# Performance work log

Measured on AMD Instinct MI355X. Metric: run time of the kernel, lower is better.

The kernel has to match this reference:

```python
import jax, jax.numpy as jnp
import numpy as np

MUL = 32          # multiplicity per irrep
NB = 10           # number_of_basis
MAX_R = 4.0
NUM_NEIGH = 16.0
NUM_NODES = 512.0
N_GRAPHS = 16
N = 8192
E = 131072
L = 3             # gated layers
C_S = float(np.sin(np.pi / 8))
C_X = float(np.cos(np.pi / 8))
SQ3 = float(np.sqrt(3.0))
SQ2 = float(np.sqrt(2.0))


def smooth_cutoff(x):
    u = 2.0 * (x - 1.0)
    y = 0.5 * (1.0 - jnp.cos(np.pi * u))
    return jnp.where(u > 0.0, 0.0, jnp.where(u < -1.0, 1.0, y))


def radial_embed(r):
    # soft_one_hot_linspace, basis='gaussian', cutoff=False, scaled by sqrt(NB)
    values = jnp.linspace(0.0, MAX_R, NB)
    step = values[1] - values[0]
    diff = (r[:, None] - values[None, :]) / step
    return jnp.exp(-diff * diff) / 1.12 * np.sqrt(NB)


def _lin_s(a, w):  # scalar-channel linear with e3nn fan-in norm
    return (a @ w) / np.sqrt(w.shape[0])


def _lin_v(a, w):  # vector-channel (l=1) linear, acts on multiplicity only
    return jnp.einsum('nui,uv->nvi', a, w) / np.sqrt(w.shape[0])


def forward(x, edge_vec, lin1_so, lin1_se, lin1_vo, lin1_ve,
            sc_so, sc_se, sc_vo, sc_ve, rad_w1, rad_w2,
            lin2_so, lin2_se, lin2_vo, lin2_ve,
            flin1_se, flin1_vo, fsc_se, frad_w1, frad_w2, flin2,
            edge_src, edge_dst, batch):
    n = x.shape[0]
    M = MUL
    # split node features into irrep blocks: 32x0o + 32x0e + 32x1o + 32x1e
    s_o = x[:, :M]
    s_e = x[:, M:2 * M]
    v_o = x[:, 2 * M:5 * M].reshape(n, M, 3)
    v_e = x[:, 5 * M:8 * M].reshape(n, M, 3)

    r = jnp.linalg.norm(edge_vec, axis=1)
    unit = edge_vec / (r[:, None] + 1e-12)
    cut = smooth_cutoff(r / MAX_R)          # [E]
    y0 = cut                                # l=0 edge attr (Y0 = 1, component norm)
    y1 = SQ3 * unit * cut[:, None]          # l=1 edge attr, [E,3]
    emb = radial_embed(r)                   # [E,NB]

    def seg(v):
        return jax.ops.segment_sum(v, edge_dst, num_segments=n) / np.sqrt(NUM_NEIGH)

    inv2 = 1.0 / np.sqrt(2.0)  # path normalization: 2 tp paths into output irrep
    inv3 = 1.0 / np.sqrt(3.0)  # 3 tp paths into output irrep

    def layer(carry, p):
        s_o, s_e, v_o, v_e = carry
        (w1so, w1se, w1vo, w1ve, wsso, wsse, wsvo, wsve,
         rw1, rw2, w2so, w2se, w2vo, w2ve) = p
        # lin1 (FullyConnectedTensorProduct with trivial node attr == per-irrep linear)
        a_so, a_se = _lin_s(s_o, w1so), _lin_s(s_e, w1se)
        a_vo, a_ve = _lin_v(v_o, w1vo), _lin_v(v_e, w1ve)
        e_so, e_se = a_so[edge_src], a_se[edge_src]
        e_vo, e_ve = a_vo[edge_src], a_ve[edge_src]
        # radial MLP -> per-edge tensor-product weights (10 uvu paths x MUL)
        h = jax.nn.silu(emb @ rw1 / np.sqrt(NB))
        w = (h @ rw2 / np.sqrt(rw1.shape[1])).reshape(-1, 10, M)
        # explicit lmax=1 Clebsch-Gordan contractions
        dot_ve = jnp.einsum('eui,ei->eu', e_ve, y1) / SQ3   # 1e x 1o -> 0o
        dot_vo = jnp.einsum('eui,ei->eu', e_vo, y1) / SQ3   # 1o x 1o -> 0e
        cr_ve = jnp.cross(e_ve, y1[:, None, :]) / SQ2       # 1e x 1o -> 1o
        cr_vo = jnp.cross(e_vo, y1[:, None, :]) / SQ2       # 1o x 1o -> 1e
        m0o = jnp.concatenate([w[:, 0] * e_so * y0[:, None],
                               w[:, 1] * dot_ve], axis=1) * inv2          # [E,2M]
        m0e = jnp.concatenate([w[:, 2] * e_se * y0[:, None],
                               w[:, 3] * dot_vo], axis=1) * inv2          # [E,2M]
        m1o = jnp.concatenate([w[:, 4][:, :, None] * e_se[:, :, None] * y1[:, None, :],
                               w[:, 5][:, :, None] * e_vo * y0[:, None, None],
                               w[:, 6][:, :, None] * cr_ve], axis=1) * inv3  # [E,3M,3]
        m1e = jnp.concatenate([w[:, 7][:, :, None] * e_so[:, :, None] * y1[:, None, :],
                               w[:, 8][:, :, None] * cr_vo,
                               w[:, 9][:, :, None] * e_ve * y0[:, None, None]], axis=1) * inv3
        n0o, n0e, n1o, n1e = seg(m0o), seg(m0e), seg(m1o), seg(m1e)
        # lin2 plus self-connection skip: sin(pi/8)*sc + cos(pi/8)*conv
        o0o = C_S * _lin_s(s_o, wsso) + C_X * _lin_s(n0o, w2so)   # [N,M]
        o0e = C_S * _lin_s(s_e, wsse) + C_X * _lin_s(n0e, w2se)   # [N,3M] (M scalars + 2M gates)
        o1o = C_S * _lin_v(v_o, wsvo) + C_X * _lin_v(n1o, w2vo)   # [N,M,3]
        o1e = C_S * _lin_v(v_e, wsve) + C_X * _lin_v(n1e, w2ve)   # [N,M,3]
        # Gate: tanh on 0o scalars, silu on 0e scalars, sigmoid gates on vectors
        ns_o = jnp.tanh(o0o)
        ns_e = jax.nn.silu(o0e[:, :M])
        g = jax.nn.sigmoid(o0e[:, M:])
        nv_o = o1o * g[:, :M, None]
        nv_e = o1e * g[:, M:, None]
        return (ns_o, ns_e, nv_o, nv_e), None

    (s_o, s_e, v_o, v_e), _ = jax.lax.scan(
        layer, (s_o, s_e, v_o, v_e),
        (lin1_so, lin1_se, lin1_vo, lin1_ve, sc_so, sc_se, sc_vo, sc_ve,
         rad_w1, rad_w2, lin2_so, lin2_se, lin2_vo, lin2_ve))

    # final convolution -> 1x0e (paths: 0e x 0e -> 0e, 1o x 1o -> 0e)
    a_se = _lin_s(s_e, flin1_se)
    a_vo = _lin_v(v_o, flin1_vo)
    h = jax.nn.silu(emb @ frad_w1 / np.sqrt(NB))
    w = (h @ frad_w2 / np.sqrt(frad_w1.shape[1])).reshape(-1, 2, MUL)
    dot_vo = jnp.einsum('eui,ei->eu', a_vo[edge_src], y1) / SQ3
    m0e = jnp.concatenate([w[:, 0] * a_se[edge_src] * y0[:, None],
                           w[:, 1] * dot_vo], axis=1) * inv2
    n0e = seg(m0e)
    out = C_S * _lin_s(s_e, fsc_se) + C_X * _lin_s(n0e, flin2)   # [N,1]
    # reduce_output: per-graph sum / sqrt(num_nodes)
    return jax.ops.segment_sum(out, batch, num_segments=N_GRAPHS) / np.sqrt(NUM_NODES)


def setup_inputs():
    key = jax.random.key(0)
    ks = jax.random.split(key, 26)
    rn = lambda k, s: jax.random.normal(k, s, dtype=jnp.float32)
    M = MUL
    return {
        "x": rn(ks[0], (N, 8 * M)),
        "edge_vec": rn(ks[1], (E, 3)),
        "lin1_so": rn(ks[2], (L, M, M)),
        "lin1_se": rn(ks[3], (L, M, M)),
        "lin1_vo": rn(ks[4], (L, M, M)),
        "lin1_ve": rn(ks[5], (L, M, M)),
        "sc_so": rn(ks[6], (L, M, M)),
        "sc_se": rn(ks[7], (L, M, 3 * M)),
        "sc_vo": rn(ks[8], (L, M, M)),
        "sc_ve": rn(ks[9], (L, M, M)),
        "rad_w1": rn(ks[10], (L, NB, 100)),
        "rad_w2": rn(ks[11], (L, 100, 10 * M)),
        "lin2_so": rn(ks[12], (L, 2 * M, M)),
        "lin2_se": rn(ks[13], (L, 2 * M, 3 * M)),
        "lin2_vo": rn(ks[14], (L, 3 * M, M)),
        "lin2_ve": rn(ks[15], (L, 3 * M, M)),
        "flin1_se": rn(ks[16], (M, M)),
        "flin1_vo": rn(ks[17], (M, M)),
        "fsc_se": rn(ks[18], (M, 1)),
        "frad_w1": rn(ks[19], (NB, 100)),
        "frad_w2": rn(ks[20], (100, 2 * M)),
        "flin2": rn(ks[21], (2 * M, 1)),
        "edge_src": jax.random.randint(ks[22], (E,), 0, N),
        "edge_dst": jax.random.randint(ks[23], (E,), 0, N),
        "batch": jnp.sort(jax.random.randint(ks[24], (N,), 0, N_GRAPHS)),
    }


def reference(x, edge_vec, lin1_so, lin1_se, lin1_vo, lin1_ve,
              sc_so, sc_se, sc_vo, sc_ve, rad_w1, rad_w2,
              lin2_so, lin2_se, lin2_vo, lin2_ve,
              flin1_se, flin1_vo, fsc_se, frad_w1, frad_w2, flin2,
              edge_src, edge_dst, batch):
    return forward(x, edge_vec, lin1_so, lin1_se, lin1_vo, lin1_ve,
                   sc_so, sc_se, sc_vo, sc_ve, rad_w1, rad_w2,
                   lin2_so, lin2_se, lin2_vo, lin2_ve,
                   flin1_se, flin1_vo, fsc_se, frad_w1, frad_w2, flin2,
                   edge_src, edge_dst, batch)
```

## Files before the change

kernel.cpp:

```cpp
#include <hip/hip_runtime.h>
#include <hip/hip_bf16.h>
#include <math.h>
#include <string.h>
#include <stdint.h>

#define NN 8192
#define EE 131072

#define PI_F     3.14159265358979323846f
#define SQRT3_F  1.7320508075688772f
#define INV_SQ2  0.7071067811865476f
#define INV_SQ3  0.5773502691896258f
#define INV_S32  0.17677669529663687f
#define INV_S96  0.10206207261596575f
#define INV_S10  0.31622776601683794f
#define C_S_F    0.3826834323650898f
#define C_X_F    0.9238795325112867f
#define EMB_S    2.8234621965789795f
#define OUT_S    0.044194173824159216f

typedef unsigned int uint;
typedef unsigned short ushort;
typedef unsigned long long u64;
typedef __attribute__((ext_vector_type(8))) short short8;
typedef __attribute__((ext_vector_type(4))) float float4v;

__device__ __forceinline__ float sigmoid_f(float x){ return 1.0f/(1.0f+__expf(-x)); }
__device__ __forceinline__ ushort f2bf(float f){
    uint u = __float_as_uint(f);
    u = (u + 0x7fffu + ((u>>16)&1u)) >> 16;
    return (ushort)u;
}
__device__ __forceinline__ float bf2f(ushort w){ return __uint_as_float(((uint)w)<<16); }
__device__ __forceinline__ uint pk2bf(float a, float b){
    __hip_bfloat162 h = __float22bfloat162_rn(make_float2(a,b));
    uint u; memcpy(&u,&h,4); return u;
}

__global__ __launch_bounds__(256) void k_count(const int* __restrict__ dst, int* __restrict__ cnt)
{
    int e = blockIdx.x*256 + threadIdx.x;
    atomicAdd(&cnt[dst[e]], 1);
}

__global__ __launch_bounds__(1024) void k_scan(const int* __restrict__ cnt,
    int* __restrict__ off, int* __restrict__ cur)
{
    __shared__ int partial[1024];
    int t = threadIdx.x;
    int base = t*8;
    int local[8];
    int s = 0;
    #pragma unroll
    for(int i=0;i<8;i++){ local[i]=s; s += cnt[base+i]; }
    partial[t] = s;
    __syncthreads();
    for(int d=1; d<1024; d<<=1){
        int v = (t>=d) ? partial[t-d] : 0;
        __syncthreads();
        partial[t] += v;
        __syncthreads();
    }
    int pref = (t>0) ? partial[t-1] : 0;
    #pragma unroll
    for(int i=0;i<8;i++){
        int o = pref + local[i];
        off[base+i] = o; cur[base+i] = o;
    }
    if (t==1023) off[NN] = partial[1023];
}

__global__ __launch_bounds__(256) void k_scatter(const int* __restrict__ dst,
    int* __restrict__ cur, int* __restrict__ eids)
{
    int e = blockIdx.x*256 + threadIdx.x;
    int p = atomicAdd(&cur[dst[e]], 1);
    eids[p] = e;
}

__global__ __launch_bounds__(256) void k_geom_sorted(const float* __restrict__ ev,
    const int* __restrict__ eids, const int* __restrict__ esrc,
    const int* __restrict__ edst, const int* __restrict__ batch,
    float* __restrict__ y0s, float* __restrict__ y1s, float* __restrict__ embs,
    int* __restrict__ esrcs, int* __restrict__ gbs)
{
    int p = blockIdx.x*256 + threadIdx.x;
    int e = eids[p];
    float vx=ev[e*3+0], vy=ev[e*3+1], vz=ev[e*3+2];
    float r = sqrtf(vx*vx+vy*vy+vz*vz);
    float uu = 0.5f*r - 2.0f;
    float cut;
    if (uu > 0.0f)       cut = 0.0f;
    else if (uu < -1.0f) cut = 1.0f;
    else                 cut = 0.5f*(1.0f - cosf(PI_F*uu));
    y0s[p] = cut;
    float s = SQRT3_F*cut/(r + 1e-12f);
    y1s[p*3+0]=vx*s; y1s[p*3+1]=vy*s; y1s[p*3+2]=vz*s;
    #pragma unroll
    for(int b=0;b<10;b++){
        float d = r*2.25f - (float)b;
        embs[p*10+b] = __expf(-d*d)*EMB_S;
    }
    esrcs[p] = esrc[e];
    gbs[p]   = batch[edst[e]];
}

__global__ __launch_bounds__(256) void k_lin1(const float* __restrict__ st,
    const float* __restrict__ w_so, const float* __restrict__ w_se,
    const float* __restrict__ w_vo, const float* __restrict__ w_ve,
    float* __restrict__ A)
{
    __shared__ float wl[4][1024];
    __shared__ float sl[8][256];
    int t = threadIdx.x;
    for(int i=t;i<1024;i+=256){ wl[0][i]=w_so[i]; wl[1][i]=w_se[i]; wl[2][i]=w_vo[i]; wl[3][i]=w_ve[i]; }
    int n0 = blockIdx.x*8;
    for(int i=t;i<2048;i+=256){ int k=i>>8, c=i&255; sl[k][c]=st[(n0+k)*256+c]; }
    __syncthreads();
    for(int k=0;k<8;k++){
        float acc = 0.0f;
        if (t < 64){
            int m = t>>5, v = t&31;
            const float* w = wl[m];
            const float* s = &sl[k][m*32];
            #pragma unroll
            for(int u=0;u<32;u++) acc += s[u]*w[u*32+v];
        } else if (t < 160){
            int idx=t-64, i=idx>>5, v=idx&31;
            #pragma unroll
            for(int u=0;u<32;u++) acc += sl[k][64+u*3+i]*wl[2][u*32+v];
        } else {
            int idx=t-160, i=idx>>5, v=idx&31;
            #pragma unroll
            for(int u=0;u<32;u++) acc += sl[k][160+u*3+i]*wl[3][u*32+v];
        }
        A[(n0+k)*256 + t] = acc * INV_S32;
    }
}

__global__ __launch_bounds__(256) void k_prep3(const float* __restrict__ rw2, ushort* __restrict__ Bfrag)
{
    int L = blockIdx.x / 160;
    int idx = (blockIdx.x % 160)*256 + threadIdx.x;
    int j = idx & 7;
    int l = (idx>>3) & 63;
    int rest = idx >> 9;
    int nt = rest % 20;
    int ks = rest / 20;
    int k = ks*32 + ((l>>4)&3)*8 + j;
    int p = nt*16 + (l&15);
    int n = (p % 10)*32 + p/10;
    float v = (k < 100) ? rw2[L*32000 + k*320 + n] : 0.0f;
    Bfrag[L*40960 + idx] = f2bf(v);
}

__global__ __launch_bounds__(256) void k_prep64(const float* __restrict__ rw2, ushort* __restrict__ Bfrag)
{
    int idx = blockIdx.x*256 + threadIdx.x;
    int j = idx & 7;
    int l = (idx>>3) & 63;
    int rest = idx >> 9;
    int nt = rest % 4;
    int ks = rest / 4;
    int k = ks*32 + ((l>>4)&3)*8 + j;
    int p = nt*16 + (l&15);
    int n = (p % 2)*32 + p/2;
    float v = (k < 100) ? rw2[k*64 + n] : 0.0f;
    Bfrag[idx] = f2bf(v);
}

__global__ __launch_bounds__(256) void k_prepu(
    const float* __restrict__ sc_so, const float* __restrict__ sc_se,
    const float* __restrict__ sc_vo, const float* __restrict__ sc_ve,
    const float* __restrict__ lin2_so, const float* __restrict__ lin2_se,
    const float* __restrict__ lin2_vo, const float* __restrict__ lin2_ve,
    float* __restrict__ Wcat0, float* __restrict__ Wcat1)
{
    int idx = blockIdx.x*256 + threadIdx.x;
    int L = idx / 20480;
    int k = idx % 20480;
    const float CS32 = C_S_F*INV_S32, CX8 = C_X_F*0.125f, CX96 = C_X_F*INV_S96;
    if (k < 12288){
        int r = k >> 7, c = k & 127;
        float v;
        if (c < 32) v = (r<32) ? CS32*sc_so[L*1024 + r*32+c]        : CX8*lin2_so[L*2048 + (r-32)*32+c];
        else        v = (r<32) ? CS32*sc_se[L*3072 + r*96+(c-32)]   : CX8*lin2_se[L*6144 + (r-32)*96+(c-32)];
        Wcat0[L*12288 + k] = v;
    } else {
        int k2 = k - 12288;
        int r = k2 >> 6, c = k2 & 63;
        float v;
        if (c < 32) v = (r<32) ? CS32*sc_vo[L*1024 + r*32+c]        : CX96*lin2_vo[L*3072 + (r-32)*32+c];
        else        v = (r<32) ? CS32*sc_ve[L*1024 + r*32+(c-32)]   : CX96*lin2_ve[L*3072 + (r-32)*32+(c-32)];
        Wcat1[L*8192 + k2] = v;
    }
}

template<int NCOL>
__global__ __launch_bounds__(256, 3) void k_radial_mfma(const float* __restrict__ emb,
    const float* __restrict__ rw1, const ushort* __restrict__ Afrag,
    ushort* __restrict__ Wout)
{
    constexpr int MTW = NCOL/64;
    __shared__ __align__(16) ushort s_frag[8192];
    __shared__ float s_emb[640];
    int t = threadIdx.x;
    int ebase = blockIdx.x*64;
    for(int i=t;i<640;i+=256)  s_emb[i] = emb[ebase*10 + i];
    for(int i=t;i<1024;i+=256) ((uint*)s_frag)[3072 + i] = 0u;
    __syncthreads();
    {
        int w4 = __builtin_amdgcn_readfirstlane(t) >> 6;
        int l = t & 63;
        float ev[10];
        #pragma unroll
        for(int r=0;r<10;r++) ev[r] = s_emb[l*10 + r];
        int m  = l & 15, nt = l >> 4;
        int kbeg = w4*25;
        #pragma unroll 5
        for(int k=kbeg; k<kbeg+25; k++){
            float a0 = 0.0f;
            #pragma unroll
            for(int r=0;r<10;r++) a0 += ev[r]*rw1[r*100 + k];
            a0 *= INV_S10;
            float h = a0*sigmoid_f(a0);
            int ks = k >> 5, kk = k & 31;
            int lt = m | ((kk>>3)<<4);
            s_frag[((ks*4 + nt)*64 + lt)*8 + (kk&7)] = f2bf(h);
        }
    }
    __syncthreads();
    int w = t >> 6, l = t & 63;
    float4v acc[MTW][4];
    #pragma unroll
    for(int a=0;a<MTW;a++)
        #pragma unroll
        for(int b=0;b<4;b++)
            acc[a][b] = (float4v){0.f,0.f,0.f,0.f};
    #pragma unroll
    for(int ks=0;ks<4;ks++){
        short8 bfr[4];
        #pragma unroll
        for(int nt=0;nt<4;nt++)
            bfr[nt] = *((const short8*)&s_frag[((ks*4+nt)*64 + l)*8]);
        #pragma unroll
        for(int mtl=0;mtl<MTW;mtl++){
            short8 af = *((const short8*)(Afrag + ((size_t)(ks*(NCOL/16) + w*MTW + mtl)*64 + l)*8));
            #pragma unroll
            for(int nt=0;nt<4;nt++)
                acc[mtl][nt] = __builtin_amdgcn_mfma_f32_16x16x32_bf16(af, bfr[nt], acc[mtl][nt], 0, 0, 0);
        }
    }
    {
        int col16 = l & 15, rquad = l >> 4;
        #pragma unroll
        for(int mtl=0;mtl<MTW;mtl++){
            int pos0 = (w*MTW + mtl)*16 + rquad*4;
            #pragma unroll
            for(int nt=0;nt<4;nt++){
                int edge = ebase + nt*16 + col16;
                uint u01 = pk2bf(acc[mtl][nt][0]*0.1f, acc[mtl][nt][1]*0.1f);
                uint u23 = pk2bf(acc[mtl][nt][2]*0.1f, acc[mtl][nt][3]*0.1f);
                u64 pk = (u64)u01 | ((u64)u23 << 32);
                *((u64*)(Wout + (size_t)edge*NCOL + pos0)) = pk;
            }
        }
    }
}

__global__ __launch_bounds__(256) void k_aggregate(const float* __restrict__ A,
    const ushort* __restrict__ W2, const float* __restrict__ y0s,
    const float* __restrict__ y1s, const int* __restrict__ off,
    const int* __restrict__ esrcs, float* __restrict__ nbuf)
{
    int t = threadIdx.x;
    int n = blockIdx.x*4 + (t >> 6);
    int l = t & 63;
    int u = l & 31, half = l >> 5;
    int e0 = off[n], e1 = off[n+1];
    float a_n0o0=0.f, a_n0o1=0.f, a_n0e0=0.f, a_n0e1=0.f;
    float a1o[3][3] = {{0}}, a1e[3][3] = {{0}};
    #pragma unroll 2
    for(int p=e0;p<e1;p+=2){
        int idx = p + half;
        bool valid = idx < e1;
        int ic = valid ? idx : e0;
        int s = esrcs[ic];
        float cy0 = valid ? y0s[ic] : 0.0f;
        float v1x = y1s[ic*3+0], v1y = y1s[ic*3+1], v1z = y1s[ic*3+2];
        if (!valid){ v1x=0.f; v1y=0.f; v1z=0.f; }
        const float* Ar = A + s*256;
        float aso=Ar[u],      ase=Ar[32+u];
        float vox=Ar[64+u],   voy=Ar[96+u],  voz=Ar[128+u];
        float vex=Ar[160+u],  vey=Ar[192+u], vez=Ar[224+u];
        const uint* Wr = (const uint*)(W2 + (size_t)ic*320 + u*10);
        uint p01=Wr[0], p23=Wr[1], p45=Wr[2], p67=Wr[3], p89=Wr[4];
        float w0=bf2f((ushort)p01), w1=bf2f((ushort)(p01>>16));
        float w2=bf2f((ushort)p23), w3=bf2f((ushort)(p23>>16));
        float w4=bf2f((ushort)p45), w5=bf2f((ushort)(p45>>16));
        float w6=bf2f((ushort)p67), w7=bf2f((ushort)(p67>>16));
        float w8=bf2f((ushort)p89), w9=bf2f((ushort)(p89>>16));
        float dve = (vex*v1x+vey*v1y+vez*v1z)*INV_SQ3;
        float dvo = (vox*v1x+voy*v1y+voz*v1z)*INV_SQ3;
        float cvex=(vey*v1z-vez*v1y)*INV_SQ2, cvey=(vez*v1x-vex*v1z)*INV_SQ2, cvez=(vex*v1y-vey*v1x)*INV_SQ2;
        float cvox=(voy*v1z-voz*v1y)*INV_SQ2, cvoy=(voz*v1x-vox*v1z)*INV_SQ2, cvoz=(vox*v1y-voy*v1x)*INV_SQ2;
        a_n0o0 += w0*aso*cy0;
        a_n0o1 += w1*dve;
        a_n0e0 += w2*ase*cy0;
        a_n0e1 += w3*dvo;
        a1o[0][0]+=w4*ase*v1x; a1o[0][1]+=w4*ase*v1y; a1o[0][2]+=w4*ase*v1z;
        a1o[1][0]+=w5*vox*cy0; a1o[1][1]+=w5*voy*cy0; a1o[1][2]+=w5*voz*cy0;
        a1o[2][0]+=w6*cvex;    a1o[2][1]+=w6*cvey;    a1o[2][2]+=w6*cvez;
        a1e[0][0]+=w7*aso*v1x; a1e[0][1]+=w7*aso*v1y; a1e[0][2]+=w7*aso*v1z;
        a1e[1][0]+=w8*cvox;    a1e[1][1]+=w8*cvoy;    a1e[1][2]+=w8*cvoz;
        a1e[2][0]+=w9*vex*cy0; a1e[2][1]+=w9*vey*cy0; a1e[2][2]+=w9*vez*cy0;
    }
    a_n0o0 += __shfl_xor(a_n0o0, 32);
    a_n0o1 += __shfl_xor(a_n0o1, 32);
    a_n0e0 += __shfl_xor(a_n0e0, 32);
    a_n0e1 += __shfl_xor(a_n0e1, 32);
    #pragma unroll
    for(int sp=0;sp<3;sp++)
        #pragma unroll
        for(int i=0;i<3;i++){
            a1o[sp][i] += __shfl_xor(a1o[sp][i], 32);
            a1e[sp][i] += __shfl_xor(a1e[sp][i], 32);
        }
    float s0 = INV_SQ2*0.25f;
    float s1 = INV_SQ3*0.25f;
    float* nb = nbuf + n*704;
    if (half==0){
        nb[u]      = a_n0o0*s0;
        nb[32+u]   = a_n0o1*s0;
        nb[64+u]   = a_n0e0*s0;
        nb[96+u]   = a_n0e1*s0;
        #pragma unroll
        for(int sp=0;sp<3;sp++)
            #pragma unroll
            for(int i=0;i<3;i++)
                nb[128 + i*96 + sp*32 + u] = a1o[sp][i]*s1;
    } else {
        #pragma unroll
        for(int sp=0;sp<3;sp++)
            #pragma unroll
            for(int i=0;i<3;i++)
                nb[416 + i*96 + sp*32 + u] = a1e[sp][i]*s1;
    }
}

__global__ __launch_bounds__(256, 4) void k_update(const float* __restrict__ st,
    const float* __restrict__ nbuf, const float* __restrict__ W0,
    const float* __restrict__ W1, float* __restrict__ stnew)
{
    __shared__ float X0T[192][8];
    __shared__ float X1T[3][256][8];
    __shared__ float G[8][64];
    int t = threadIdx.x;
    int n0 = blockIdx.x*8;
    for (int idx=t; idx<2048; idx+=256){
        int nb = idx>>8, c = idx&255;
        float v = st[(n0+nb)*256 + c];
        if (c<32)       X0T[c][nb]=v;
        else if (c<64)  X0T[96+(c-32)][nb]=v;
        else if (c<160){ int cc=c-64;  X1T[cc%3][cc/3][nb]=v; }
        else           { int cc=c-160; X1T[cc%3][128+cc/3][nb]=v; }
    }
    for (int idx=t; idx<5632; idx+=256){
        int nb = idx/704, o = idx%704;
        float v = nbuf[(n0+nb)*704 + o];
        if (o<64)       X0T[32+o][nb]=v;
        else if (o<128) X0T[128+(o-64)][nb]=v;
        else if (o<416){ int oo=o-128; X1T[oo/96][32+(oo%96)][nb]=v; }
        else           { int oo=o-416; X1T[oo/96][160+(oo%96)][nb]=v; }
    }
    __syncthreads();
    {
        int c = t & 127, h = t >> 7;
        float a0=0.f,a1=0.f,a2=0.f,a3=0.f;
        int qb = (c<32) ? 0 : 96;
        #pragma unroll 4
        for (int r=0;r<96;r++){
            float w = W0[r*128+c];
            const float* xp = &X0T[qb+r][h*4];
            a0 += w*xp[0]; a1 += w*xp[1]; a2 += w*xp[2]; a3 += w*xp[3];
        }
        float accs[4]={a0,a1,a2,a3};
        #pragma unroll
        for (int j=0;j<4;j++){
            int nb = h*4+j, n = n0+nb;
            float o = accs[j];
            if (c<32)       stnew[n*256+c] = tanhf(o);
            else if (c<64)  stnew[n*256+c] = o*sigmoid_f(o);
            else            G[nb][c-64] = sigmoid_f(o);
        }
    }
    __syncthreads();
    int c2 = t & 63, w = t >> 6;
    if (w < 3){
        float acc[8];
        #pragma unroll
        for(int j=0;j<8;j++) acc[j]=0.f;
        int qb = (c2<32) ? 0 : 128;
        #pragma unroll 2
        for (int r=0;r<128;r++){
            float wt = W1[r*64+c2];
            const float* xp = &X1T[w][qb+r][0];
            #pragma unroll
            for(int j=0;j<8;j++) acc[j] += wt*xp[j];
        }
        int base = (c2<32) ? 64 + c2*3 + w : 160 + (c2-32)*3 + w;
        #pragma unroll
        for(int j=0;j<8;j++)
            stnew[(n0+j)*256 + base] = acc[j]*G[j][c2];
    }
}

__global__ __launch_bounds__(128) void k_flin(const float* __restrict__ st,
    const float* __restrict__ wse, const float* __restrict__ wvo,
    const float* __restrict__ fsc_se,
    float* __restrict__ afin, float* __restrict__ sk)
{
    int n = blockIdx.x, t = threadIdx.x;
    const float* sr = st + n*256;
    float acc = 0.0f;
    if (t < 32){
        #pragma unroll
        for(int u=0;u<32;u++) acc += sr[32+u]*wse[u*32+t];
    } else {
        int idx=t-32, i=idx>>5, v=idx&31;
        #pragma unroll
        for(int u=0;u<32;u++) acc += sr[64+u*3+i]*wvo[u*32+v];
    }
    afin[n*128 + t] = acc * INV_S32;
    if (t < 32){
        float v = sr[32+t]*fsc_se[t];
        #pragma unroll
        for(int o=16;o>0;o>>=1) v += __shfl_xor(v, o);
        if (t==0) sk[n] = v * (C_S_F*INV_S32*OUT_S);
    }
}

__global__ __launch_bounds__(256) void k_fagg(const float* __restrict__ afin,
    const ushort* __restrict__ Wf2, const int* __restrict__ esrcs,
    const float* __restrict__ y0s, const float* __restrict__ y1s,
    const int* __restrict__ gbs, const float* __restrict__ flin2,
    float* __restrict__ fpart)
{
    __shared__ float s_g[16];
    int t = threadIdx.x;
    if (t < 16) s_g[t] = 0.0f;
    __syncthreads();
    int u = t & 31, half = (t>>5)&1, w = t >> 6;
    const float FACT = C_X_F*0.125f*INV_SQ2*0.25f*OUT_S;
    float fl0 = flin2[u], fl1 = flin2[32+u];
    int base = (blockIdx.x*4 + w)*64;
    #pragma unroll 2
    for(int it=0; it<32; it++){
        int idx = base + it*2 + half;
        int s = esrcs[idx];
        float cy0 = y0s[idx];
        float v1x=y1s[idx*3+0], v1y=y1s[idx*3+1], v1z=y1s[idx*3+2];
        const float* Ar = afin + s*128;
        float ase = Ar[u];
        float vx=Ar[32+u], vy=Ar[64+u], vz=Ar[96+u];
        uint p01 = *((const uint*)(Wf2 + (size_t)idx*64 + u*2));
        float w0 = bf2f((ushort)p01), w1 = bf2f((ushort)(p01>>16));
        float val = fl0*w0*ase*cy0 + fl1*w1*((vx*v1x+vy*v1y+vz*v1z)*INV_SQ3);
        #pragma unroll
        for(int o=16;o>0;o>>=1) val += __shfl_xor(val, o);
        if (u==0) atomicAdd(&s_g[gbs[idx]], val*FACT);
    }
    __syncthreads();
    if (t < 16) fpart[blockIdx.x*16 + t] = s_g[t];
}

__global__ __launch_bounds__(256) void k_final(const float* __restrict__ sk,
    const int* __restrict__ batch, const float* __restrict__ fpart,
    float* __restrict__ out)
{
    __shared__ float bins[16];
    int t = threadIdx.x, b = blockIdx.x;
    if (t < 16) bins[t] = 0.0f;
    __syncthreads();
    if (t < 128){
        int n = b*128 + t;
        atomicAdd(&bins[batch[n]], sk[n]);
    } else {
        int i = b*128 + (t-128);
        atomicAdd(&bins[i & 15], fpart[i]);
    }
    __syncthreads();
    if (t < 16) atomicAdd(&out[t], bins[t]);
}

extern "C" void kernel_launch(void* const* d_in, const int* in_sizes, int n_in,
                              void* d_out, int out_size, void* d_ws, size_t ws_size,
                              hipStream_t stream)
{
    const float* x        = (const float*)d_in[0];
    const float* edge_vec = (const float*)d_in[1];
    const float* lin1_so  = (const float*)d_in[2];
    const float* lin1_se  = (const float*)d_in[3];
    const float* lin1_vo  = (const float*)d_in[4];
    const float* lin1_ve  = (const float*)d_in[5];
    const float* sc_so    = (const float*)d_in[6];
    const float* sc_se    = (const float*)d_in[7];
    const float* sc_vo    = (const float*)d_in[8];
    const float* sc_ve    = (const float*)d_in[9];
    const float* rad_w1   = (const float*)d_in[10];
    const float* rad_w2   = (const float*)d_in[11];
    const float* lin2_so  = (const float*)d_in[12];
    const float* lin2_se  = (const float*)d_in[13];
    const float* lin2_vo  = (const float*)d_in[14];
    const float* lin2_ve  = (const float*)d_in[15];
    const float* flin1_se = (const float*)d_in[16];
    const float* flin1_vo = (const float*)d_in[17];
    const float* fsc_se   = (const float*)d_in[18];
    const float* frad_w1  = (const float*)d_in[19];
    const float* frad_w2  = (const float*)d_in[20];
    const float* flin2    = (const float*)d_in[21];
    const int*   esrc     = (const int*)d_in[22];
    const int*   edst     = (const int*)d_in[23];
    const int*   batch    = (const int*)d_in[24];
    float* out = (float*)d_out;

    uint8_t* ws = (uint8_t*)d_ws;
    size_t off = 0;
    auto alloc = [&](size_t bytes)->void* {
        void* p = ws + off;
        off += (bytes + 255) & ~(size_t)255;
        return p;
    };
    float* y0s   = (float*)alloc((size_t)EE*4);
    float* y1s   = (float*)alloc((size_t)EE*12);
    float* embs  = (float*)alloc((size_t)EE*40);
    int*   esrcs = (int*)  alloc((size_t)EE*4);
    int*   gbs   = (int*)  alloc((size_t)EE*4);
    int*   cnt   = (int*)  alloc((size_t)NN*4);
    int*   csro  = (int*)  alloc((size_t)(NN+1)*4);
    int*   cur   = (int*)  alloc((size_t)NN*4);
    int*   eids  = (int*)  alloc((size_t)EE*4);
    float* A     = (float*)alloc((size_t)NN*256*4);
    ushort* W    = (ushort*)alloc((size_t)EE*320*2);
    ushort* Bfrag3=(ushort*)alloc((size_t)3*40960*2);
    ushort* BfragF=(ushort*)alloc((size_t)8192*2);
    float* Wcat0 = (float*)alloc((size_t)3*12288*4);
    float* Wcat1 = (float*)alloc((size_t)3*8192*4);
    float* nbuf  = (float*)alloc((size_t)NN*704*4);
    float* st0   = (float*)alloc((size_t)NN*256*4);
    float* st1   = (float*)alloc((size_t)NN*256*4);
    float* afin  = (float*)alloc((size_t)NN*128*4);
    float* sk    = (float*)alloc((size_t)NN*4);
    float* fpart = (float*)alloc((size_t)512*16*4);

    hipMemsetAsync(out, 0, (size_t)out_size*sizeof(float), stream);
    hipMemsetAsync(cnt, 0, (size_t)NN*4, stream);

    k_count  <<<EE/256, 256, 0, stream>>>(edst, cnt);
    k_scan   <<<1, 1024, 0, stream>>>(cnt, csro, cur);
    k_scatter<<<EE/256, 256, 0, stream>>>(edst, cur, eids);
    k_geom_sorted<<<EE/256, 256, 0, stream>>>(edge_vec, eids, esrc, edst, batch,
                                              y0s, y1s, embs, esrcs, gbs);
    k_prep3<<<480, 256, 0, stream>>>(rad_w2, Bfrag3);
    k_prep64<<<32, 256, 0, stream>>>(frad_w2, BfragF);
    k_prepu<<<240, 256, 0, stream>>>(sc_so, sc_se, sc_vo, sc_ve,
                                     lin2_so, lin2_se, lin2_vo, lin2_ve, Wcat0, Wcat1);

    const float* st_in = x;
    float* bufs[2] = { st0, st1 };
    for (int l=0; l<3; l++){
        k_lin1<<<NN/8, 256, 0, stream>>>(st_in,
            lin1_so + l*1024, lin1_se + l*1024, lin1_vo + l*1024, lin1_ve + l*1024, A);
        k_radial_mfma<320><<<EE/64, 256, 0, stream>>>(embs, rad_w1 + l*1000, Bfrag3 + l*40960, W);
        k_aggregate<<<NN/4, 256, 0, stream>>>(A, W, y0s, y1s, csro, esrcs, nbuf);
        float* st_out = bufs[l & 1];
        k_update<<<NN/8, 256, 0, stream>>>(st_in, nbuf, Wcat0 + l*12288, Wcat1 + l*8192, st_out);
        st_in = st_out;
    }
    k_flin<<<NN, 128, 0, stream>>>(st_in, flin1_se, flin1_vo, fsc_se, afin, sk);
    k_radial_mfma<64><<<EE/64, 256, 0, stream>>>(embs, frad_w1, BfragF, W);
    k_fagg<<<512, 256, 0, stream>>>(afin, W, esrcs, y0s, y1s, gbs, flin2, fpart);
    k_final<<<64, 256, 0, stream>>>(sk, batch, fpart, out);
}
```

Measured before the change: 578.0 us.

## Pack edge geometry into float4 and permute radial weight layout for coalescing

Edge geometry (cutoff plus the three l=1 components) is merged into one float4 per edge, so the aggregate and final-aggregate kernels issue a single vector load instead of four scalar loads. The column permutation in the radial weight prep is changed so each edge's per-channel bf16 weight pairs are laid out channel-contiguous, and the aggregate kernel's five weight loads become coalesced across lanes instead of strided by 10. The aggregate kernel also moves to one 64-thread block per node instead of four nodes per 256-thread block, which may help balance uneven degrees but adds more, smaller blocks.

Result: no change. 583.8 us (+1.0%).

```diff
diff --git a/kernel.cpp b/kernel.cpp
--- a/kernel.cpp
+++ b/kernel.cpp
@@ -81,7 +81,7 @@
 __global__ __launch_bounds__(256) void k_geom_sorted(const float* __restrict__ ev,
     const int* __restrict__ eids, const int* __restrict__ esrc,
     const int* __restrict__ edst, const int* __restrict__ batch,
-    float* __restrict__ y0s, float* __restrict__ y1s, float* __restrict__ embs,
+    float4* __restrict__ ygeo, float* __restrict__ embs,
     int* __restrict__ esrcs, int* __restrict__ gbs)
 {
     int p = blockIdx.x*256 + threadIdx.x;
@@ -93,9 +93,8 @@
     if (uu > 0.0f)       cut = 0.0f;
     else if (uu < -1.0f) cut = 1.0f;
     else                 cut = 0.5f*(1.0f - cosf(PI_F*uu));
-    y0s[p] = cut;
     float s = SQRT3_F*cut/(r + 1e-12f);
-    y1s[p*3+0]=vx*s; y1s[p*3+1]=vy*s; y1s[p*3+2]=vz*s;
+    ygeo[p] = make_float4(cut, vx*s, vy*s, vz*s);
     #pragma unroll
     for(int b=0;b<10;b++){
         float d = r*2.25f - (float)b;
@@ -149,7 +148,7 @@
     int ks = rest / 20;
     int k = ks*32 + ((l>>4)&3)*8 + j;
     int p = nt*16 + (l&15);
-    int n = (p % 10)*32 + p/10;
+    int n = (2*(p>>6) + (p&1))*32 + ((p&63)>>1);
     float v = (k < 100) ? rw2[L*32000 + k*320 + n] : 0.0f;
     Bfrag[L*40960 + idx] = f2bf(v);
 }
@@ -268,14 +267,13 @@
     }
 }
 
-__global__ __launch_bounds__(256) void k_aggregate(const float* __restrict__ A,
-    const ushort* __restrict__ W2, const float* __restrict__ y0s,
-    const float* __restrict__ y1s, const int* __restrict__ off,
-    const int* __restrict__ esrcs, float* __restrict__ nbuf)
-{
-    int t = threadIdx.x;
-    int n = blockIdx.x*4 + (t >> 6);
-    int l = t & 63;
+__global__ __launch_bounds__(64) void k_aggregate(const float* __restrict__ A,
+    const ushort* __restrict__ W2, const float4* __restrict__ ygeo,
+    const int* __restrict__ off, const int* __restrict__ esrcs,
+    float* __restrict__ nbuf)
+{
+    int n = blockIdx.x;
+    int l = threadIdx.x;
     int u = l & 31, half = l >> 5;
     int e0 = off[n], e1 = off[n+1];
     float a_n0o0=0.f, a_n0o1=0.f, a_n0e0=0.f, a_n0e1=0.f;
@@ -286,15 +284,16 @@
         bool valid = idx < e1;
         int ic = valid ? idx : e0;
         int s = esrcs[ic];
-        float cy0 = valid ? y0s[ic] : 0.0f;
-        float v1x = y1s[ic*3+0], v1y = y1s[ic*3+1], v1z = y1s[ic*3+2];
+        float4 yg = ygeo[ic];
+        float cy0 = valid ? yg.x : 0.0f;
+        float v1x = yg.y, v1y = yg.z, v1z = yg.w;
         if (!valid){ v1x=0.f; v1y=0.f; v1z=0.f; }
         const float* Ar = A + s*256;
         float aso=Ar[u],      ase=Ar[32+u];
         float vox=Ar[64+u],   voy=Ar[96+u],  voz=Ar[128+u];
         float vex=Ar[160+u],  vey=Ar[192+u], vez=Ar[224+u];
-        const uint* Wr = (const uint*)(W2 + (size_t)ic*320 + u*10);
-        uint p01=Wr[0], p23=Wr[1], p45=Wr[2], p67=Wr[3], p89=Wr[4];
+        const uint* Wu = (const uint*)(W2) + (size_t)ic*160;
+        uint p01=Wu[u], p23=Wu[32+u], p45=Wu[64+u], p67=Wu[96+u], p89=Wu[128+u];
         float w0=bf2f((ushort)p01), w1=bf2f((ushort)(p01>>16));
         float w2=bf2f((ushort)p23), w3=bf2f((ushort)(p23>>16));
         float w4=bf2f((ushort)p45), w5=bf2f((ushort)(p45>>16));
@@ -442,9 +441,8 @@
 
 __global__ __launch_bounds__(256) void k_fagg(const float* __restrict__ afin,
     const ushort* __restrict__ Wf2, const int* __restrict__ esrcs,
-    const float* __restrict__ y0s, const float* __restrict__ y1s,
-    const int* __restrict__ gbs, const float* __restrict__ flin2,
-    float* __restrict__ fpart)
+    const float4* __restrict__ ygeo, const int* __restrict__ gbs,
+    const float* __restrict__ flin2, float* __restrict__ fpart)
 {
     __shared__ float s_g[16];
     int t = threadIdx.x;
@@ -458,14 +456,13 @@
     for(int it=0; it<32; it++){
         int idx = base + it*2 + half;
         int s = esrcs[idx];
-        float cy0 = y0s[idx];
-        float v1x=y1s[idx*3+0], v1y=y1s[idx*3+1], v1z=y1s[idx*3+2];
+        float4 yg = ygeo[idx];
         const float* Ar = afin + s*128;
         float ase = Ar[u];
         float vx=Ar[32+u], vy=Ar[64+u], vz=Ar[96+u];
         uint p01 = *((const uint*)(Wf2 + (size_t)idx*64 + u*2));
         float w0 = bf2f((ushort)p01), w1 = bf2f((ushort)(p01>>16));
-        float val = fl0*w0*ase*cy0 + fl1*w1*((vx*v1x+vy*v1y+vz*v1z)*INV_SQ3);
+        float val = fl0*w0*ase*yg.x + fl1*w1*((vx*yg.y+vy*yg.z+vz*yg.w)*INV_SQ3);
         #pragma unroll
         for(int o=16;o>0;o>>=1) val += __shfl_xor(val, o);
         if (u==0) atomicAdd(&s_g[gbs[idx]], val*FACT);
@@ -531,8 +528,7 @@
         off += (bytes + 255) & ~(size_t)255;
         return p;
     };
-    float* y0s   = (float*)alloc((size_t)EE*4);
-    float* y1s   = (float*)alloc((size_t)EE*12);
+    float4* ygeo = (float4*)alloc((size_t)EE*16);
     float* embs  = (float*)alloc((size_t)EE*40);
     int*   esrcs = (int*)  alloc((size_t)EE*4);
     int*   gbs   = (int*)  alloc((size_t)EE*4);
@@ -560,7 +556,7 @@
     k_scan   <<<1, 1024, 0, stream>>>(cnt, csro, cur);
     k_scatter<<<EE/256, 256, 0, stream>>>(edst, cur, eids);
     k_geom_sorted<<<EE/256, 256, 0, stream>>>(edge_vec, eids, esrc, edst, batch,
-                                              y0s, y1s, embs, esrcs, gbs);
+                                              ygeo, embs, esrcs, gbs);
     k_prep3<<<480, 256, 0, stream>>>(rad_w2, Bfrag3);
     k_prep64<<<32, 256, 0, stream>>>(frad_w2, BfragF);
     k_prepu<<<240, 256, 0, stream>>>(sc_so, sc_se, sc_vo, sc_ve,
@@ -572,13 +568,13 @@
         k_lin1<<<NN/8, 256, 0, stream>>>(st_in,
             lin1_so + l*1024, lin1_se + l*1024, lin1_vo + l*1024, lin1_ve + l*1024, A);
         k_radial_mfma<320><<<EE/64, 256, 0, stream>>>(embs, rad_w1 + l*1000, Bfrag3 + l*40960, W);
-        k_aggregate<<<NN/4, 256, 0, stream>>>(A, W, y0s, y1s, csro, esrcs, nbuf);
+        k_aggregate<<<NN, 64, 0, stream>>>(A, W, ygeo, csro, esrcs, nbuf);
         float* st_out = bufs[l & 1];
         k_update<<<NN/8, 256, 0, stream>>>(st_in, nbuf, Wcat0 + l*12288, Wcat1 + l*8192, st_out);
         st_in = st_out;
     }
     k_flin<<<NN, 128, 0, stream>>>(st_in, flin1_se, flin1_vo, fsc_se, afin, sk);
     k_radial_mfma<64><<<EE/64, 256, 0, stream>>>(embs, frad_w1, BfragF, W);
-    k_fagg<<<512, 256, 0, stream>>>(afin, W, esrcs, y0s, y1s, gbs, flin2, fpart);
+    k_fagg<<<512, 256, 0, stream>>>(afin, W, esrcs, ygeo, gbs, flin2, fpart);
     k_final<<<64, 256, 0, stream>>>(sk, batch, fpart, out);
 }
```
